# Optimization experiments

Hardware: AMD Instinct MI355X
Metric: run time of the kernel (lower is better)

## Reference

```python
import jax, jax.numpy as jnp
import numpy as np

B, T, D, H = 2, 4096, 768, 12
HD = D // H  # head_dim = 64


def setup_inputs() -> dict:
    key = jax.random.key(0)
    ks = jax.random.split(key, 6)
    s = 0.02
    return {
        "x": jax.random.normal(ks[0], (B, T, D), dtype=jnp.float32),
        "Wq": jax.random.normal(ks[1], (D, D), dtype=jnp.float32) * s,
        "Wk": jax.random.normal(ks[2], (D, D), dtype=jnp.float32) * s,
        "Wv": jax.random.normal(ks[3], (D, D), dtype=jnp.float32) * s,
        "Wo": jax.random.normal(ks[4], (D, D), dtype=jnp.float32) * s,
        "bo": jnp.zeros((D,), dtype=jnp.float32),
    }


def reference(x, Wq, Wk, Wv, Wo, bo):
    b, t, d = x.shape
    # QKV projections (no bias), reshape to [B, H, T, HD]
    def heads(w):
        return (x @ w.T).reshape(b, t, H, HD).transpose(0, 2, 1, 3)
    q, k, v = heads(Wq), heads(Wk), heads(Wv)
    scores = jnp.einsum("bhqd,bhkd->bhqk", q, k)  # [B,H,T,T]
    causal = jnp.tril(jnp.ones((t, t), dtype=bool))
    scores = jnp.where(causal, scores, -jnp.inf)
    attn = jax.nn.softmax(scores / jnp.sqrt(jnp.float32(HD)), axis=-1)
    ctx = jnp.einsum("bhqk,bhkd->bhqd", attn, v)  # [B,H,T,HD]
    ctx = ctx.transpose(0, 2, 1, 3).reshape(b, t, d)
    return ctx @ Wo.T + bo
```

## Files before the change

kernel.cpp:

```cpp
#include <hip/hip_runtime.h>
#include <hip/hip_bf16.h>
#include <cstdint>
#include <cstddef>

#define B_  2
#define T_  4096
#define D_  768
#define H_  12
#define HD_ 64
#define M_  (B_*T_)

#define SCL 0.18033688f

typedef __bf16 bf16x8 __attribute__((ext_vector_type(8)));
typedef float  f32x4  __attribute__((ext_vector_type(4)));
using bf16 = __hip_bfloat16;

__device__ inline float fexp2(float x) {
  float r; asm("v_exp_f32 %0, %1" : "=v"(r) : "v"(x)); return r;
}
__device__ inline uint32_t fu(float x) { union { float f; uint32_t u; } c; c.f = x; return c.u; }
__device__ inline uint32_t pktr(float a, float b) {
  return __builtin_amdgcn_perm(fu(b), fu(a), 0x07060302);
}
#define GLD16(g, l) __builtin_amdgcn_global_load_lds( \
    (const __attribute__((address_space(1))) uint32_t*)(const void*)(g), \
    (__attribute__((address_space(3))) uint32_t*)(void*)(l), 16, 0, 0)

__global__ void cvt_all(const float* __restrict__ x,
                        const float* __restrict__ w0, const float* __restrict__ w1,
                        const float* __restrict__ w2, const float* __restrict__ w3,
                        bf16* __restrict__ xd,
                        bf16* __restrict__ d0, bf16* __restrict__ d1,
                        bf16* __restrict__ d2, bf16* __restrict__ d3) {
  const float* s; bf16* d; int n4;
  switch (blockIdx.y) {
    case 0: s = x;  d = xd; n4 = M_ * D_ / 4; break;
    case 1: s = w0; d = d0; n4 = D_ * D_ / 4; break;
    case 2: s = w1; d = d1; n4 = D_ * D_ / 4; break;
    case 3: s = w2; d = d2; n4 = D_ * D_ / 4; break;
    default: s = w3; d = d3; n4 = D_ * D_ / 4; break;
  }
  int i = blockIdx.x * blockDim.x + threadIdx.x;
  if (i < n4) {
    float4 v = ((const float4*)s)[i];
    union { bf16 o[4]; uint2 u; } pk;
    pk.o[0] = __float2bfloat16(v.x); pk.o[1] = __float2bfloat16(v.y);
    pk.o[2] = __float2bfloat16(v.z); pk.o[3] = __float2bfloat16(v.w);
    *(uint2*)(d + 4 * (size_t)i) = pk.u;
  }
}

__global__ __launch_bounds__(256) void gemm_qkv(const bf16* __restrict__ A,
                                                const bf16* __restrict__ W0,
                                                const bf16* __restrict__ W1,
                                                const bf16* __restrict__ W2,
                                                bf16* __restrict__ O0,
                                                bf16* __restrict__ O1,
                                                bf16* __restrict__ O2t) {
  __shared__ bf16 As[2][4096];
  __shared__ bf16 Bs[2][4096];
  const int z = blockIdx.z;
  const char* Bw = (const char*)((z == 0) ? W0 : ((z == 1) ? W1 : W2));
  const char* Ap = (const char*)A;
  const int t  = threadIdx.x;
  const int m0 = blockIdx.y * 128;
  const int n0 = blockIdx.x * 128;
  const int w = t >> 6, lane = t & 63;
  const int wm = (w >> 1) * 64, wn = (w & 1) * 64;
  const int mi = lane & 15, qd = lane >> 4;

  int aoff[2], boff[2];
  #pragma unroll
  for (int i = 0; i < 2; ++i) {
    int L = i * 256 + t;
    int row = L >> 2, sl = L & 3, c = sl ^ (row & 3);
    aoff[i] = (m0 + row) * 1536 + c * 16;
    boff[i] = (n0 + row) * 1536 + c * 16;
  }
  const int fsw = (qd ^ (mi & 3)) * 8;

  f32x4 acc[4][4] = {};

  #pragma unroll
  for (int i = 0; i < 2; ++i) {
    GLD16(Ap + aoff[i], &As[0][i * 2048 + w * 512]);
    GLD16(Bw + boff[i], &Bs[0][i * 2048 + w * 512]);
  }

  for (int kk = 0; kk < 24; ++kk) {
    __syncthreads();
    const int par = kk & 1;
    if (kk + 1 < 24) {
      const int np = par ^ 1, kb = (kk + 1) * 64;
      #pragma unroll
      for (int i = 0; i < 2; ++i) {
        GLD16(Ap + aoff[i] + kb, &As[np][i * 2048 + w * 512]);
        GLD16(Bw + boff[i] + kb, &Bs[np][i * 2048 + w * 512]);
      }
    }
    bf16x8 af[4], bfr[4];
    #pragma unroll
    for (int mt = 0; mt < 4; ++mt)
      af[mt] = *(const bf16x8*)&As[par][(wm + mt * 16 + mi) * 32 + fsw];
    #pragma unroll
    for (int nt = 0; nt < 4; ++nt)
      bfr[nt] = *(const bf16x8*)&Bs[par][(wn + nt * 16 + mi) * 32 + fsw];
    #pragma unroll
    for (int mt = 0; mt < 4; ++mt)
      #pragma unroll
      for (int nt = 0; nt < 4; ++nt)
        acc[mt][nt] = __builtin_amdgcn_mfma_f32_16x16x32_bf16(af[mt], bfr[nt], acc[mt][nt], 0, 0, 0);
  }

  const float scl = (z == 1) ? SCL : 1.0f;
  bf16* Ob = (z == 0) ? O0 : O1;
  #pragma unroll
  for (int mt = 0; mt < 4; ++mt) {
    #pragma unroll
    for (int nt = 0; nt < 4; ++nt) {
      int gr0 = m0 + wm + mt * 16 + qd * 4;
      int gc  = n0 + wn + nt * 16 + mi;
      if (z == 2) {
        union { bf16 o[4]; uint2 u; } pk;
        #pragma unroll
        for (int r = 0; r < 4; ++r) pk.o[r] = __float2bfloat16(acc[mt][nt][r]);
        int bb = gr0 >> 12, tt = gr0 & 4095;
        *(uint2*)(O2t + (size_t)bb * 768 * 4096 + (size_t)gc * 4096 + tt) = pk.u;
      } else {
        #pragma unroll
        for (int r = 0; r < 4; ++r)
          Ob[(size_t)(gr0 + r) * 768 + gc] = __float2bfloat16(acc[mt][nt][r] * scl);
      }
    }
  }
}

__global__ __launch_bounds__(256) void gemm_out(const bf16* __restrict__ A,
                                                const bf16* __restrict__ Bw0,
                                                float* __restrict__ Cf,
                                                const float* __restrict__ bias) {
  __shared__ bf16 As[2][4096];
  __shared__ bf16 Bs[2][4096];
  const char* Ap = (const char*)A;
  const char* Bw = (const char*)Bw0;
  const int t  = threadIdx.x;
  const int m0 = blockIdx.y * 128;
  const int n0 = blockIdx.x * 128;
  const int w = t >> 6, lane = t & 63;
  const int wm = (w >> 1) * 64, wn = (w & 1) * 64;
  const int mi = lane & 15, qd = lane >> 4;

  int aoff[2], boff[2];
  #pragma unroll
  for (int i = 0; i < 2; ++i) {
    int L = i * 256 + t;
    int row = L >> 2, sl = L & 3, c = sl ^ (row & 3);
    aoff[i] = (m0 + row) * 1536 + c * 16;
    boff[i] = (n0 + row) * 1536 + c * 16;
  }
  const int fsw = (qd ^ (mi & 3)) * 8;

  f32x4 acc[4][4] = {};

  #pragma unroll
  for (int i = 0; i < 2; ++i) {
    GLD16(Ap + aoff[i], &As[0][i * 2048 + w * 512]);
    GLD16(Bw + boff[i], &Bs[0][i * 2048 + w * 512]);
  }

  for (int kk = 0; kk < 24; ++kk) {
    __syncthreads();
    const int par = kk & 1;
    if (kk + 1 < 24) {
      const int np = par ^ 1, kb = (kk + 1) * 64;
      #pragma unroll
      for (int i = 0; i < 2; ++i) {
        GLD16(Ap + aoff[i] + kb, &As[np][i * 2048 + w * 512]);
        GLD16(Bw + boff[i] + kb, &Bs[np][i * 2048 + w * 512]);
      }
    }
    bf16x8 af[4], bfr[4];
    #pragma unroll
    for (int mt = 0; mt < 4; ++mt)
      af[mt] = *(const bf16x8*)&As[par][(wm + mt * 16 + mi) * 32 + fsw];
    #pragma unroll
    for (int nt = 0; nt < 4; ++nt)
      bfr[nt] = *(const bf16x8*)&Bs[par][(wn + nt * 16 + mi) * 32 + fsw];
    #pragma unroll
    for (int mt = 0; mt < 4; ++mt)
      #pragma unroll
      for (int nt = 0; nt < 4; ++nt)
        acc[mt][nt] = __builtin_amdgcn_mfma_f32_16x16x32_bf16(af[mt], bfr[nt], acc[mt][nt], 0, 0, 0);
  }

  #pragma unroll
  for (int mt = 0; mt < 4; ++mt)
    #pragma unroll
    for (int nt = 0; nt < 4; ++nt) {
      int gr0 = m0 + wm + mt * 16 + qd * 4;
      int gc  = n0 + wn + nt * 16 + mi;
      #pragma unroll
      for (int r = 0; r < 4; ++r)
        Cf[(size_t)(gr0 + r) * 768 + gc] = acc[mt][nt][r] + bias[gc];
    }
}

__global__ __launch_bounds__(256) void flash_attn(const bf16* __restrict__ Q,
                                                  const bf16* __restrict__ K,
                                                  const bf16* __restrict__ Vt,
                                                  bf16* __restrict__ ctx) {
  __shared__ bf16 Ks[2][4096];
  __shared__ bf16 Vs[2][4096];
  __shared__ bf16 Pt[4][32 * 72];
  const int t = threadIdx.x;
  const int w = t >> 6, lane = t & 63;
  const int mi = lane & 15, qd = lane >> 4;
  const int bh   = blockIdx.x % 24;
  const int qrev = blockIdx.x / 24;
  const int q0 = T_ - 128 - qrev * 128;
  const int b = bh / H_, h = bh % H_;
  const size_t bTD = (size_t)b * T_ * D_;
  const char* Kp = (const char*)(K  + bTD + (size_t)h * HD_);
  const char* Vp = (const char*)(Vt + (size_t)b * D_ * T_ + (size_t)h * HD_ * T_);
  const int qwmin = q0 + w * 32;

  int vkoff[2], vvoff[2];
  #pragma unroll
  for (int i = 0; i < 2; ++i) {
    int s  = i * 64 + lane;
    int rl = s >> 3, cs = s & 7;
    int c  = cs ^ (rl & 7);
    vkoff[i] = (w * 16 + rl) * 1536 + c * 16;
    vvoff[i] = (w * 16 + rl) * 8192 + c * 16;
  }

  int fidx[4][2];
  #pragma unroll
  for (int jt = 0; jt < 4; ++jt)
    #pragma unroll
    for (int kt = 0; kt < 2; ++kt)
      fidx[jt][kt] = (jt * 16 + mi) * 64 + (((kt * 4 + qd) ^ (mi & 7)) * 8);

  bf16x8 qf[2][2];
  const bf16* Qp = Q + bTD + (size_t)h * HD_;
  #pragma unroll
  for (int qt = 0; qt < 2; ++qt)
    #pragma unroll
    for (int kt = 0; kt < 2; ++kt)
      qf[qt][kt] = *(const bf16x8*)(Qp + (size_t)(qwmin + qt * 16 + mi) * D_ + kt * 32 + qd * 8);

  f32x4 oacc[4][2] = {};
  float lst[2] = {0.f, 0.f};

  const int ntiles = q0 / 64 + 2;

  #pragma unroll
  for (int i = 0; i < 2; ++i) {
    GLD16(Kp + vkoff[i], &Ks[0][w * 1024 + i * 512]);
    GLD16(Vp + vvoff[i], &Vs[0][w * 1024 + i * 512]);
  }

  for (int tt = 0; tt < ntiles; ++tt) {
    __syncthreads();
    const int par = tt & 1;
    if (tt + 1 < ntiles) {
      const size_t j1 = (size_t)(tt + 1) * 64;
      const int np = par ^ 1;
      #pragma unroll
      for (int i = 0; i < 2; ++i) {
        GLD16(Kp + vkoff[i] + j1 * 1536, &Ks[np][w * 1024 + i * 512]);
        GLD16(Vp + vvoff[i] + j1 * 2,    &Vs[np][w * 1024 + i * 512]);
      }
    }
    const int j0 = tt * 64;
    if (j0 > qwmin + 31) continue;

    f32x4 sacc[4][2] = {};
    #pragma unroll
    for (int jt = 0; jt < 4; ++jt)
      #pragma unroll
      for (int kt = 0; kt < 2; ++kt) {
        bf16x8 kf = *(const bf16x8*)&Ks[par][fidx[jt][kt]];
        #pragma unroll
        for (int qt = 0; qt < 2; ++qt)
          sacc[jt][qt] = __builtin_amdgcn_mfma_f32_16x16x32_bf16(kf, qf[qt][kt], sacc[jt][qt], 0, 0, 0);
      }

    if (j0 + 63 > qwmin) {
      #pragma unroll
      for (int jt = 0; jt < 4; ++jt)
        #pragma unroll
        for (int qt = 0; qt < 2; ++qt) {
          int qg = qwmin + qt * 16 + mi;
          #pragma unroll
          for (int r = 0; r < 4; ++r) {
            int jg = j0 + jt * 16 + qd * 4 + r;
            if (jg > qg) sacc[jt][qt][r] = -1e30f;
          }
        }
    }

    #pragma unroll
    for (int jt = 0; jt < 4; ++jt)
      #pragma unroll
      for (int qt = 0; qt < 2; ++qt) {
        float p0 = fexp2(sacc[jt][qt][0]);
        float p1 = fexp2(sacc[jt][qt][1]);
        float p2 = fexp2(sacc[jt][qt][2]);
        float p3 = fexp2(sacc[jt][qt][3]);
        lst[qt] += (p0 + p1) + (p2 + p3);
        union { uint32_t u[2]; uint64_t d; } pw;
        pw.u[0] = pktr(p0, p1);
        pw.u[1] = pktr(p2, p3);
        *(uint64_t*)&Pt[w][(qt * 16 + mi) * 72 + jt * 16 + qd * 4] = pw.d;
      }

    bf16x8 vf[4][2];
    #pragma unroll
    for (int dt = 0; dt < 4; ++dt)
      #pragma unroll
      for (int kt = 0; kt < 2; ++kt)
        vf[dt][kt] = *(const bf16x8*)&Vs[par][fidx[dt][kt]];

    asm volatile("s_waitcnt lgkmcnt(0)" ::: "memory");

    #pragma unroll
    for (int ktp = 0; ktp < 2; ++ktp)
      #pragma unroll
      for (int qt = 0; qt < 2; ++qt) {
        bf16x8 pf = *(const bf16x8*)&Pt[w][(qt * 16 + mi) * 72 + ktp * 32 + qd * 8];
        #pragma unroll
        for (int dt = 0; dt < 4; ++dt)
          oacc[dt][qt] = __builtin_amdgcn_mfma_f32_16x16x32_bf16(vf[dt][ktp], pf, oacc[dt][qt], 0, 0, 0);
      }
  }

  #pragma unroll
  for (int qt = 0; qt < 2; ++qt) {
    float l = lst[qt];
    l += __shfl_xor(l, 16);
    l += __shfl_xor(l, 32);
    float inv = __builtin_amdgcn_rcpf(l);
    int qg = qwmin + qt * 16 + mi;
    bf16* cp = ctx + bTD + (size_t)qg * D_ + h * HD_ + qd * 4;
    #pragma unroll
    for (int dt = 0; dt < 4; ++dt) {
      union { bf16 o[4]; uint2 u; } pko;
      #pragma unroll
      for (int r = 0; r < 4; ++r) pko.o[r] = __float2bfloat16(oacc[dt][qt][r] * inv);
      *(uint2*)(cp + dt * 16) = pko.u;
    }
  }
}

extern "C" void kernel_launch(void* const* d_in, const int* in_sizes, int n_in,
                              void* d_out, int out_size, void* d_ws, size_t ws_size,
                              hipStream_t stream) {
  const float* x  = (const float*)d_in[0];
  const float* Wq = (const float*)d_in[1];
  const float* Wk = (const float*)d_in[2];
  const float* Wv = (const float*)d_in[3];
  const float* Wo = (const float*)d_in[4];
  const float* bo = (const float*)d_in[5];
  float* out = (float*)d_out;

  char* ws = (char*)d_ws;
  const size_t SZ  = (size_t)M_ * D_ * 2;
  const size_t WSZ = (size_t)D_ * D_ * 2;
  bf16* xb   = (bf16*)(ws);
  bf16* Qb   = (bf16*)(ws + 1 * SZ);
  bf16* Kb   = (bf16*)(ws + 2 * SZ);
  bf16* Vtg  = (bf16*)(ws + 3 * SZ);
  bf16* ctxb = (bf16*)(ws + 4 * SZ);
  bf16* Wqb  = (bf16*)(ws + 5 * SZ);
  bf16* Wkb  = (bf16*)(ws + 5 * SZ + 1 * WSZ);
  bf16* Wvb  = (bf16*)(ws + 5 * SZ + 2 * WSZ);
  bf16* Wob  = (bf16*)(ws + 5 * SZ + 3 * WSZ);

  dim3 gcv(M_ * D_ / 4 / 256, 5);
  cvt_all<<<gcv, 256, 0, stream>>>(x, Wq, Wk, Wv, Wo, xb, Wqb, Wkb, Wvb, Wob);

  dim3 gq(D_ / 128, M_ / 128, 3);
  gemm_qkv<<<gq, 256, 0, stream>>>(xb, Wqb, Wkb, Wvb, Qb, Kb, Vtg);

  flash_attn<<<(T_ / 128) * B_ * H_, 256, 0, stream>>>(Qb, Kb, Vtg, ctxb);

  dim3 gg(D_ / 128, M_ / 128);
  gemm_out<<<gg, 256, 0, stream>>>(ctxb, Wob, out, bo);
}
```

Baseline: 266.0 us.

## Keep P in registers via 16x16x16 MFMA, compact convert grid, vectorize GEMM stores

The flash attention P·V product now uses the 16x16x16 bf16 MFMA, whose operand layout matches the score accumulator, so probabilities stay in registers instead of round-tripping through LDS with a wait. The conversion kernel launches a compact 1D grid instead of a 5-row grid in which most weight blocks exit early. The Q/K and output GEMMs swap MFMA operands so each lane holds contiguous output columns, which allows 8-byte bf16 and 16-byte float4 stores with a vectorized bias load. The trade-off is twice as many, smaller MFMA instructions in the P·V loop.

```diff
diff --git a/kernel.cpp b/kernel.cpp
--- a/kernel.cpp
+++ b/kernel.cpp
@@ -14,7 +14,10 @@
 
 typedef __bf16 bf16x8 __attribute__((ext_vector_type(8)));
 typedef float  f32x4  __attribute__((ext_vector_type(4)));
+typedef short  s16x4  __attribute__((ext_vector_type(4)));
 using bf16 = __hip_bfloat16;
+
+#define HAS_MFMA16 __has_builtin(__builtin_amdgcn_mfma_f32_16x16x16bf16_1k)
 
 __device__ inline float fexp2(float x) {
   float r; asm("v_exp_f32 %0, %1" : "=v"(r) : "v"(x)); return r;
@@ -33,22 +36,25 @@
                         bf16* __restrict__ xd,
                         bf16* __restrict__ d0, bf16* __restrict__ d1,
                         bf16* __restrict__ d2, bf16* __restrict__ d3) {
-  const float* s; bf16* d; int n4;
-  switch (blockIdx.y) {
-    case 0: s = x;  d = xd; n4 = M_ * D_ / 4; break;
-    case 1: s = w0; d = d0; n4 = D_ * D_ / 4; break;
-    case 2: s = w1; d = d1; n4 = D_ * D_ / 4; break;
-    case 3: s = w2; d = d2; n4 = D_ * D_ / 4; break;
-    default: s = w3; d = d3; n4 = D_ * D_ / 4; break;
-  }
-  int i = blockIdx.x * blockDim.x + threadIdx.x;
-  if (i < n4) {
-    float4 v = ((const float4*)s)[i];
-    union { bf16 o[4]; uint2 u; } pk;
-    pk.o[0] = __float2bfloat16(v.x); pk.o[1] = __float2bfloat16(v.y);
-    pk.o[2] = __float2bfloat16(v.z); pk.o[3] = __float2bfloat16(v.w);
-    *(uint2*)(d + 4 * (size_t)i) = pk.u;
-  }
+  int blk = blockIdx.x;
+  const float* s; bf16* d; int i;
+  if (blk < 6144) {
+    s = x; d = xd; i = blk * 256 + threadIdx.x;
+  } else {
+    int q = blk - 6144, which = q / 576, rb = q % 576;
+    switch (which) {
+      case 0: s = w0; d = d0; break;
+      case 1: s = w1; d = d1; break;
+      case 2: s = w2; d = d2; break;
+      default: s = w3; d = d3; break;
+    }
+    i = rb * 256 + threadIdx.x;
+  }
+  float4 v = ((const float4*)s)[i];
+  union { bf16 o[4]; uint2 u; } pk;
+  pk.o[0] = __float2bfloat16(v.x); pk.o[1] = __float2bfloat16(v.y);
+  pk.o[2] = __float2bfloat16(v.z); pk.o[3] = __float2bfloat16(v.w);
+  *(uint2*)(d + 4 * (size_t)i) = pk.u;
 }
 
 __global__ __launch_bounds__(256) void gemm_qkv(const bf16* __restrict__ A,
@@ -106,33 +112,48 @@
     #pragma unroll
     for (int nt = 0; nt < 4; ++nt)
       bfr[nt] = *(const bf16x8*)&Bs[par][(wn + nt * 16 + mi) * 32 + fsw];
+    if (z == 2) {
+      #pragma unroll
+      for (int mt = 0; mt < 4; ++mt)
+        #pragma unroll
+        for (int nt = 0; nt < 4; ++nt)
+          acc[mt][nt] = __builtin_amdgcn_mfma_f32_16x16x32_bf16(af[mt], bfr[nt], acc[mt][nt], 0, 0, 0);
+    } else {
+      #pragma unroll
+      for (int mt = 0; mt < 4; ++mt)
+        #pragma unroll
+        for (int nt = 0; nt < 4; ++nt)
+          acc[mt][nt] = __builtin_amdgcn_mfma_f32_16x16x32_bf16(bfr[nt], af[mt], acc[mt][nt], 0, 0, 0);
+    }
+  }
+
+  if (z == 2) {
     #pragma unroll
     for (int mt = 0; mt < 4; ++mt)
       #pragma unroll
-      for (int nt = 0; nt < 4; ++nt)
-        acc[mt][nt] = __builtin_amdgcn_mfma_f32_16x16x32_bf16(af[mt], bfr[nt], acc[mt][nt], 0, 0, 0);
-  }
-
-  const float scl = (z == 1) ? SCL : 1.0f;
-  bf16* Ob = (z == 0) ? O0 : O1;
-  #pragma unroll
-  for (int mt = 0; mt < 4; ++mt) {
-    #pragma unroll
-    for (int nt = 0; nt < 4; ++nt) {
-      int gr0 = m0 + wm + mt * 16 + qd * 4;
-      int gc  = n0 + wn + nt * 16 + mi;
-      if (z == 2) {
+      for (int nt = 0; nt < 4; ++nt) {
+        int gr0 = m0 + wm + mt * 16 + qd * 4;
+        int gc  = n0 + wn + nt * 16 + mi;
         union { bf16 o[4]; uint2 u; } pk;
         #pragma unroll
         for (int r = 0; r < 4; ++r) pk.o[r] = __float2bfloat16(acc[mt][nt][r]);
         int bb = gr0 >> 12, tt = gr0 & 4095;
         *(uint2*)(O2t + (size_t)bb * 768 * 4096 + (size_t)gc * 4096 + tt) = pk.u;
-      } else {
-        #pragma unroll
-        for (int r = 0; r < 4; ++r)
-          Ob[(size_t)(gr0 + r) * 768 + gc] = __float2bfloat16(acc[mt][nt][r] * scl);
-      }
-    }
+      }
+  } else {
+    const float scl = (z == 1) ? SCL : 1.0f;
+    bf16* Ob = (z == 0) ? O0 : O1;
+    #pragma unroll
+    for (int mt = 0; mt < 4; ++mt)
+      #pragma unroll
+      for (int nt = 0; nt < 4; ++nt) {
+        int tkn = m0 + wm + mt * 16 + mi;
+        int f0  = n0 + wn + nt * 16 + qd * 4;
+        union { bf16 o[4]; uint2 u; } pk;
+        #pragma unroll
+        for (int r = 0; r < 4; ++r) pk.o[r] = __float2bfloat16(acc[mt][nt][r] * scl);
+        *(uint2*)(Ob + (size_t)tkn * 768 + f0) = pk.u;
+      }
   }
 }
 
@@ -191,18 +212,20 @@
     for (int mt = 0; mt < 4; ++mt)
       #pragma unroll
       for (int nt = 0; nt < 4; ++nt)
-        acc[mt][nt] = __builtin_amdgcn_mfma_f32_16x16x32_bf16(af[mt], bfr[nt], acc[mt][nt], 0, 0, 0);
+        acc[mt][nt] = __builtin_amdgcn_mfma_f32_16x16x32_bf16(bfr[nt], af[mt], acc[mt][nt], 0, 0, 0);
   }
 
   #pragma unroll
   for (int mt = 0; mt < 4; ++mt)
     #pragma unroll
     for (int nt = 0; nt < 4; ++nt) {
-      int gr0 = m0 + wm + mt * 16 + qd * 4;
-      int gc  = n0 + wn + nt * 16 + mi;
-      #pragma unroll
-      for (int r = 0; r < 4; ++r)
-        Cf[(size_t)(gr0 + r) * 768 + gc] = acc[mt][nt][r] + bias[gc];
+      int tkn = m0 + wm + mt * 16 + mi;
+      int f0  = n0 + wn + nt * 16 + qd * 4;
+      float4 bv = *(const float4*)&bias[f0];
+      float4 o;
+      o.x = acc[mt][nt][0] + bv.x; o.y = acc[mt][nt][1] + bv.y;
+      o.z = acc[mt][nt][2] + bv.z; o.w = acc[mt][nt][3] + bv.w;
+      *(float4*)&Cf[(size_t)tkn * 768 + f0] = o;
     }
 }
 
@@ -212,7 +235,9 @@
                                                   bf16* __restrict__ ctx) {
   __shared__ bf16 Ks[2][4096];
   __shared__ bf16 Vs[2][4096];
+#if !HAS_MFMA16
   __shared__ bf16 Pt[4][32 * 72];
+#endif
   const int t = threadIdx.x;
   const int w = t >> 6, lane = t & 63;
   const int mi = lane & 15, qd = lane >> 4;
@@ -242,6 +267,13 @@
     for (int kt = 0; kt < 2; ++kt)
       fidx[jt][kt] = (jt * 16 + mi) * 64 + (((kt * 4 + qd) ^ (mi & 7)) * 8);
 
+  int vidx[4][4];
+  #pragma unroll
+  for (int dt = 0; dt < 4; ++dt)
+    #pragma unroll
+    for (int jt = 0; jt < 4; ++jt)
+      vidx[dt][jt] = (dt * 16 + mi) * 64 + ((2 * jt + (qd >> 1)) ^ (mi & 7)) * 8 + (qd & 1) * 4;
+
   bf16x8 qf[2][2];
   const bf16* Qp = Q + bTD + (size_t)h * HD_;
   #pragma unroll
@@ -301,6 +333,7 @@
         }
     }
 
+    union { uint32_t u[2]; uint64_t d; s16x4 s; } pf[4][2];
     #pragma unroll
     for (int jt = 0; jt < 4; ++jt)
       #pragma unroll
@@ -310,30 +343,47 @@
         float p2 = fexp2(sacc[jt][qt][2]);
         float p3 = fexp2(sacc[jt][qt][3]);
         lst[qt] += (p0 + p1) + (p2 + p3);
-        union { uint32_t u[2]; uint64_t d; } pw;
-        pw.u[0] = pktr(p0, p1);
-        pw.u[1] = pktr(p2, p3);
-        *(uint64_t*)&Pt[w][(qt * 16 + mi) * 72 + jt * 16 + qd * 4] = pw.d;
-      }
-
+        pf[jt][qt].u[0] = pktr(p0, p1);
+        pf[jt][qt].u[1] = pktr(p2, p3);
+      }
+
+#if HAS_MFMA16
+    s16x4 vf4[4][4];
+    #pragma unroll
+    for (int dt = 0; dt < 4; ++dt)
+      #pragma unroll
+      for (int jt = 0; jt < 4; ++jt)
+        vf4[dt][jt] = *(const s16x4*)&Vs[par][vidx[dt][jt]];
+    #pragma unroll
+    for (int qt = 0; qt < 2; ++qt)
+      #pragma unroll
+      for (int dt = 0; dt < 4; ++dt)
+        #pragma unroll
+        for (int jt = 0; jt < 4; ++jt)
+          oacc[dt][qt] = __builtin_amdgcn_mfma_f32_16x16x16bf16_1k(vf4[dt][jt], pf[jt][qt].s, oacc[dt][qt], 0, 0, 0);
+#else
+    #pragma unroll
+    for (int jt = 0; jt < 4; ++jt)
+      #pragma unroll
+      for (int qt = 0; qt < 2; ++qt)
+        *(uint64_t*)&Pt[w][(qt * 16 + mi) * 72 + jt * 16 + qd * 4] = pf[jt][qt].d;
     bf16x8 vf[4][2];
     #pragma unroll
     for (int dt = 0; dt < 4; ++dt)
       #pragma unroll
       for (int kt = 0; kt < 2; ++kt)
         vf[dt][kt] = *(const bf16x8*)&Vs[par][fidx[dt][kt]];
-
     asm volatile("s_waitcnt lgkmcnt(0)" ::: "memory");
-
     #pragma unroll
     for (int ktp = 0; ktp < 2; ++ktp)
       #pragma unroll
       for (int qt = 0; qt < 2; ++qt) {
-        bf16x8 pf = *(const bf16x8*)&Pt[w][(qt * 16 + mi) * 72 + ktp * 32 + qd * 8];
+        bf16x8 pfx = *(const bf16x8*)&Pt[w][(qt * 16 + mi) * 72 + ktp * 32 + qd * 8];
         #pragma unroll
         for (int dt = 0; dt < 4; ++dt)
-          oacc[dt][qt] = __builtin_amdgcn_mfma_f32_16x16x32_bf16(vf[dt][ktp], pf, oacc[dt][qt], 0, 0, 0);
-      }
+          oacc[dt][qt] = __builtin_amdgcn_mfma_f32_16x16x32_bf16(vf[dt][ktp], pfx, oacc[dt][qt], 0, 0, 0);
+      }
+#endif
   }
 
   #pragma unroll
@@ -378,8 +428,7 @@
   bf16* Wvb  = (bf16*)(ws + 5 * SZ + 2 * WSZ);
   bf16* Wob  = (bf16*)(ws + 5 * SZ + 3 * WSZ);
 
-  dim3 gcv(M_ * D_ / 4 / 256, 5);
-  cvt_all<<<gcv, 256, 0, stream>>>(x, Wq, Wk, Wv, Wo, xb, Wqb, Wkb, Wvb, Wob);
+  cvt_all<<<6144 + 4 * 576, 256, 0, stream>>>(x, Wq, Wk, Wv, Wo, xb, Wqb, Wkb, Wvb, Wob);
 
   dim3 gq(D_ / 128, M_ / 128, 3);
   gemm_qkv<<<gq, 256, 0, stream>>>(xb, Wqb, Wkb, Wvb, Qb, Kb, Vtg);
```

New measurement: 281.4 us. 1.06x slower.

## Flatten grids, transpose GEMM operands for vector stores, widen attention to 512 threads

Applied to the files above, without the earlier changes.

The conversion kernel now uses a compact 1D grid, replacing the 5-row grid that wasted blocks on the small weight matrices. The QKV and output GEMMs swap operand roles (weights as A, activations as B) so each lane's accumulator holds four contiguous features, which allows packed 64-bit bf16 and float4 stores instead of scalar ones. Flash attention moves to 512 threads with 8 waves of 16 query rows each, halving per-wave register state and the K/V staging per thread. The cost is more waves sharing each K/V tile and less reuse of each K/V fragment per MFMA.

```diff
diff --git a/kernel.cpp b/kernel.cpp
--- a/kernel.cpp
+++ b/kernel.cpp
@@ -33,25 +33,28 @@
                         bf16* __restrict__ xd,
                         bf16* __restrict__ d0, bf16* __restrict__ d1,
                         bf16* __restrict__ d2, bf16* __restrict__ d3) {
-  const float* s; bf16* d; int n4;
-  switch (blockIdx.y) {
-    case 0: s = x;  d = xd; n4 = M_ * D_ / 4; break;
-    case 1: s = w0; d = d0; n4 = D_ * D_ / 4; break;
-    case 2: s = w1; d = d1; n4 = D_ * D_ / 4; break;
-    case 3: s = w2; d = d2; n4 = D_ * D_ / 4; break;
-    default: s = w3; d = d3; n4 = D_ * D_ / 4; break;
-  }
-  int i = blockIdx.x * blockDim.x + threadIdx.x;
-  if (i < n4) {
-    float4 v = ((const float4*)s)[i];
-    union { bf16 o[4]; uint2 u; } pk;
-    pk.o[0] = __float2bfloat16(v.x); pk.o[1] = __float2bfloat16(v.y);
-    pk.o[2] = __float2bfloat16(v.z); pk.o[3] = __float2bfloat16(v.w);
-    *(uint2*)(d + 4 * (size_t)i) = pk.u;
-  }
-}
-
-__global__ __launch_bounds__(256) void gemm_qkv(const bf16* __restrict__ A,
+  int blk = blockIdx.x;
+  const float* s; bf16* d; int i;
+  if (blk < 6144) {
+    s = x; d = xd; i = blk * 256 + threadIdx.x;
+  } else {
+    int q = blk - 6144, which = q / 576, rb = q % 576;
+    switch (which) {
+      case 0: s = w0; d = d0; break;
+      case 1: s = w1; d = d1; break;
+      case 2: s = w2; d = d2; break;
+      default: s = w3; d = d3; break;
+    }
+    i = rb * 256 + threadIdx.x;
+  }
+  float4 v = ((const float4*)s)[i];
+  union { bf16 o[4]; uint2 u; } pk;
+  pk.o[0] = __float2bfloat16(v.x); pk.o[1] = __float2bfloat16(v.y);
+  pk.o[2] = __float2bfloat16(v.z); pk.o[3] = __float2bfloat16(v.w);
+  *(uint2*)(d + 4 * (size_t)i) = pk.u;
+}
+
+__global__ __launch_bounds__(256) void gemm_qkv(const bf16* __restrict__ x,
                                                 const bf16* __restrict__ W0,
                                                 const bf16* __restrict__ W1,
                                                 const bf16* __restrict__ W2,
@@ -60,14 +63,18 @@
                                                 bf16* __restrict__ O2t) {
   __shared__ bf16 As[2][4096];
   __shared__ bf16 Bs[2][4096];
-  const int z = blockIdx.z;
-  const char* Bw = (const char*)((z == 0) ? W0 : ((z == 1) ? W1 : W2));
-  const char* Ap = (const char*)A;
-  const int t  = threadIdx.x;
-  const int m0 = blockIdx.y * 128;
-  const int n0 = blockIdx.x * 128;
+  const int flat = blockIdx.x;
+  const int by = flat / 18;
+  const int rr = flat % 18;
+  const int z  = rr / 6;
+  const int bx = rr % 6;
+  const bf16* Wz = (z == 0) ? W0 : ((z == 1) ? W1 : W2);
+  const char* Ap; const char* Bp; int a0, b0;
+  if (z == 2) { Ap = (const char*)x;  a0 = by * 128; Bp = (const char*)Wz; b0 = bx * 128; }
+  else        { Ap = (const char*)Wz; a0 = bx * 128; Bp = (const char*)x;  b0 = by * 128; }
+  const int t = threadIdx.x;
   const int w = t >> 6, lane = t & 63;
-  const int wm = (w >> 1) * 64, wn = (w & 1) * 64;
+  const int wa = (w >> 1) * 64, wb = (w & 1) * 64;
   const int mi = lane & 15, qd = lane >> 4;
 
   int aoff[2], boff[2];
@@ -75,8 +82,8 @@
   for (int i = 0; i < 2; ++i) {
     int L = i * 256 + t;
     int row = L >> 2, sl = L & 3, c = sl ^ (row & 3);
-    aoff[i] = (m0 + row) * 1536 + c * 16;
-    boff[i] = (n0 + row) * 1536 + c * 16;
+    aoff[i] = (a0 + row) * 1536 + c * 16;
+    boff[i] = (b0 + row) * 1536 + c * 16;
   }
   const int fsw = (qd ^ (mi & 3)) * 8;
 
@@ -85,7 +92,7 @@
   #pragma unroll
   for (int i = 0; i < 2; ++i) {
     GLD16(Ap + aoff[i], &As[0][i * 2048 + w * 512]);
-    GLD16(Bw + boff[i], &Bs[0][i * 2048 + w * 512]);
+    GLD16(Bp + boff[i], &Bs[0][i * 2048 + w * 512]);
   }
 
   for (int kk = 0; kk < 24; ++kk) {
@@ -96,59 +103,66 @@
       #pragma unroll
       for (int i = 0; i < 2; ++i) {
         GLD16(Ap + aoff[i] + kb, &As[np][i * 2048 + w * 512]);
-        GLD16(Bw + boff[i] + kb, &Bs[np][i * 2048 + w * 512]);
+        GLD16(Bp + boff[i] + kb, &Bs[np][i * 2048 + w * 512]);
       }
     }
     bf16x8 af[4], bfr[4];
     #pragma unroll
-    for (int mt = 0; mt < 4; ++mt)
-      af[mt] = *(const bf16x8*)&As[par][(wm + mt * 16 + mi) * 32 + fsw];
-    #pragma unroll
-    for (int nt = 0; nt < 4; ++nt)
-      bfr[nt] = *(const bf16x8*)&Bs[par][(wn + nt * 16 + mi) * 32 + fsw];
-    #pragma unroll
-    for (int mt = 0; mt < 4; ++mt)
-      #pragma unroll
-      for (int nt = 0; nt < 4; ++nt)
-        acc[mt][nt] = __builtin_amdgcn_mfma_f32_16x16x32_bf16(af[mt], bfr[nt], acc[mt][nt], 0, 0, 0);
-  }
-
-  const float scl = (z == 1) ? SCL : 1.0f;
-  bf16* Ob = (z == 0) ? O0 : O1;
-  #pragma unroll
-  for (int mt = 0; mt < 4; ++mt) {
-    #pragma unroll
-    for (int nt = 0; nt < 4; ++nt) {
-      int gr0 = m0 + wm + mt * 16 + qd * 4;
-      int gc  = n0 + wn + nt * 16 + mi;
-      if (z == 2) {
+    for (int at = 0; at < 4; ++at)
+      af[at] = *(const bf16x8*)&As[par][(wa + at * 16 + mi) * 32 + fsw];
+    #pragma unroll
+    for (int bt = 0; bt < 4; ++bt)
+      bfr[bt] = *(const bf16x8*)&Bs[par][(wb + bt * 16 + mi) * 32 + fsw];
+    #pragma unroll
+    for (int at = 0; at < 4; ++at)
+      #pragma unroll
+      for (int bt = 0; bt < 4; ++bt)
+        acc[at][bt] = __builtin_amdgcn_mfma_f32_16x16x32_bf16(af[at], bfr[bt], acc[at][bt], 0, 0, 0);
+  }
+
+  if (z == 2) {
+    #pragma unroll
+    for (int at = 0; at < 4; ++at)
+      #pragma unroll
+      for (int bt = 0; bt < 4; ++bt) {
+        int gr = a0 + wa + at * 16 + qd * 4;
+        int gc = b0 + wb + bt * 16 + mi;
         union { bf16 o[4]; uint2 u; } pk;
         #pragma unroll
-        for (int r = 0; r < 4; ++r) pk.o[r] = __float2bfloat16(acc[mt][nt][r]);
-        int bb = gr0 >> 12, tt = gr0 & 4095;
+        for (int r = 0; r < 4; ++r) pk.o[r] = __float2bfloat16(acc[at][bt][r]);
+        int bb = gr >> 12, tt = gr & 4095;
         *(uint2*)(O2t + (size_t)bb * 768 * 4096 + (size_t)gc * 4096 + tt) = pk.u;
-      } else {
+      }
+  } else {
+    const float scl = (z == 1) ? SCL : 1.0f;
+    bf16* Ob = (z == 0) ? O0 : O1;
+    #pragma unroll
+    for (int at = 0; at < 4; ++at)
+      #pragma unroll
+      for (int bt = 0; bt < 4; ++bt) {
+        int f0  = a0 + wa + at * 16 + qd * 4;
+        int tkn = b0 + wb + bt * 16 + mi;
+        union { bf16 o[4]; uint2 u; } pk;
         #pragma unroll
-        for (int r = 0; r < 4; ++r)
-          Ob[(size_t)(gr0 + r) * 768 + gc] = __float2bfloat16(acc[mt][nt][r] * scl);
-      }
-    }
-  }
-}
-
-__global__ __launch_bounds__(256) void gemm_out(const bf16* __restrict__ A,
-                                                const bf16* __restrict__ Bw0,
+        for (int r = 0; r < 4; ++r) pk.o[r] = __float2bfloat16(acc[at][bt][r] * scl);
+        *(uint2*)(Ob + (size_t)tkn * 768 + f0) = pk.u;
+      }
+  }
+}
+
+__global__ __launch_bounds__(256) void gemm_out(const bf16* __restrict__ ctx,
+                                                const bf16* __restrict__ Wo,
                                                 float* __restrict__ Cf,
                                                 const float* __restrict__ bias) {
   __shared__ bf16 As[2][4096];
   __shared__ bf16 Bs[2][4096];
-  const char* Ap = (const char*)A;
-  const char* Bw = (const char*)Bw0;
-  const int t  = threadIdx.x;
-  const int m0 = blockIdx.y * 128;
-  const int n0 = blockIdx.x * 128;
+  const int flat = blockIdx.x;
+  const int by = flat / 6, bx = flat % 6;
+  const char* Ap = (const char*)Wo;  const int a0 = bx * 128;
+  const char* Bp = (const char*)ctx; const int b0 = by * 128;
+  const int t = threadIdx.x;
   const int w = t >> 6, lane = t & 63;
-  const int wm = (w >> 1) * 64, wn = (w & 1) * 64;
+  const int wa = (w >> 1) * 64, wb = (w & 1) * 64;
   const int mi = lane & 15, qd = lane >> 4;
 
   int aoff[2], boff[2];
@@ -156,8 +170,8 @@
   for (int i = 0; i < 2; ++i) {
     int L = i * 256 + t;
     int row = L >> 2, sl = L & 3, c = sl ^ (row & 3);
-    aoff[i] = (m0 + row) * 1536 + c * 16;
-    boff[i] = (n0 + row) * 1536 + c * 16;
+    aoff[i] = (a0 + row) * 1536 + c * 16;
+    boff[i] = (b0 + row) * 1536 + c * 16;
   }
   const int fsw = (qd ^ (mi & 3)) * 8;
 
@@ -166,7 +180,7 @@
   #pragma unroll
   for (int i = 0; i < 2; ++i) {
     GLD16(Ap + aoff[i], &As[0][i * 2048 + w * 512]);
-    GLD16(Bw + boff[i], &Bs[0][i * 2048 + w * 512]);
+    GLD16(Bp + boff[i], &Bs[0][i * 2048 + w * 512]);
   }
 
   for (int kk = 0; kk < 24; ++kk) {
@@ -177,42 +191,44 @@
       #pragma unroll
       for (int i = 0; i < 2; ++i) {
         GLD16(Ap + aoff[i] + kb, &As[np][i * 2048 + w * 512]);
-        GLD16(Bw + boff[i] + kb, &Bs[np][i * 2048 + w * 512]);
+        GLD16(Bp + boff[i] + kb, &Bs[np][i * 2048 + w * 512]);
       }
     }
     bf16x8 af[4], bfr[4];
     #pragma unroll
-    for (int mt = 0; mt < 4; ++mt)
-      af[mt] = *(const bf16x8*)&As[par][(wm + mt * 16 + mi) * 32 + fsw];
-    #pragma unroll
-    for (int nt = 0; nt < 4; ++nt)
-      bfr[nt] = *(const bf16x8*)&Bs[par][(wn + nt * 16 + mi) * 32 + fsw];
-    #pragma unroll
-    for (int mt = 0; mt < 4; ++mt)
-      #pragma unroll
-      for (int nt = 0; nt < 4; ++nt)
-        acc[mt][nt] = __builtin_amdgcn_mfma_f32_16x16x32_bf16(af[mt], bfr[nt], acc[mt][nt], 0, 0, 0);
-  }
-
-  #pragma unroll
-  for (int mt = 0; mt < 4; ++mt)
-    #pragma unroll
-    for (int nt = 0; nt < 4; ++nt) {
-      int gr0 = m0 + wm + mt * 16 + qd * 4;
-      int gc  = n0 + wn + nt * 16 + mi;
-      #pragma unroll
-      for (int r = 0; r < 4; ++r)
-        Cf[(size_t)(gr0 + r) * 768 + gc] = acc[mt][nt][r] + bias[gc];
-    }
-}
-
-__global__ __launch_bounds__(256) void flash_attn(const bf16* __restrict__ Q,
-                                                  const bf16* __restrict__ K,
-                                                  const bf16* __restrict__ Vt,
-                                                  bf16* __restrict__ ctx) {
+    for (int at = 0; at < 4; ++at)
+      af[at] = *(const bf16x8*)&As[par][(wa + at * 16 + mi) * 32 + fsw];
+    #pragma unroll
+    for (int bt = 0; bt < 4; ++bt)
+      bfr[bt] = *(const bf16x8*)&Bs[par][(wb + bt * 16 + mi) * 32 + fsw];
+    #pragma unroll
+    for (int at = 0; at < 4; ++at)
+      #pragma unroll
+      for (int bt = 0; bt < 4; ++bt)
+        acc[at][bt] = __builtin_amdgcn_mfma_f32_16x16x32_bf16(af[at], bfr[bt], acc[at][bt], 0, 0, 0);
+  }
+
+  #pragma unroll
+  for (int at = 0; at < 4; ++at)
+    #pragma unroll
+    for (int bt = 0; bt < 4; ++bt) {
+      int f0  = a0 + wa + at * 16 + qd * 4;
+      int tkn = b0 + wb + bt * 16 + mi;
+      float4 bv = *(const float4*)&bias[f0];
+      float4 o;
+      o.x = acc[at][bt][0] + bv.x; o.y = acc[at][bt][1] + bv.y;
+      o.z = acc[at][bt][2] + bv.z; o.w = acc[at][bt][3] + bv.w;
+      *(float4*)&Cf[(size_t)tkn * 768 + f0] = o;
+    }
+}
+
+__global__ __launch_bounds__(512, 4) void flash_attn(const bf16* __restrict__ Q,
+                                                     const bf16* __restrict__ K,
+                                                     const bf16* __restrict__ Vt,
+                                                     bf16* __restrict__ ctx) {
   __shared__ bf16 Ks[2][4096];
   __shared__ bf16 Vs[2][4096];
-  __shared__ bf16 Pt[4][32 * 72];
+  __shared__ bf16 Pt[8][16 * 72];
   const int t = threadIdx.x;
   const int w = t >> 6, lane = t & 63;
   const int mi = lane & 15, qd = lane >> 4;
@@ -223,17 +239,11 @@
   const size_t bTD = (size_t)b * T_ * D_;
   const char* Kp = (const char*)(K  + bTD + (size_t)h * HD_);
   const char* Vp = (const char*)(Vt + (size_t)b * D_ * T_ + (size_t)h * HD_ * T_);
-  const int qwmin = q0 + w * 32;
-
-  int vkoff[2], vvoff[2];
-  #pragma unroll
-  for (int i = 0; i < 2; ++i) {
-    int s  = i * 64 + lane;
-    int rl = s >> 3, cs = s & 7;
-    int c  = cs ^ (rl & 7);
-    vkoff[i] = (w * 16 + rl) * 1536 + c * 16;
-    vvoff[i] = (w * 16 + rl) * 8192 + c * 16;
-  }
+  const int qw = q0 + w * 16;
+
+  const int rl = t >> 3, c = (t & 7) ^ (rl & 7);
+  const int vkoff = rl * 1536 + c * 16;
+  const int vvoff = rl * 8192 + c * 16;
 
   int fidx[4][2];
   #pragma unroll
@@ -242,24 +252,18 @@
     for (int kt = 0; kt < 2; ++kt)
       fidx[jt][kt] = (jt * 16 + mi) * 64 + (((kt * 4 + qd) ^ (mi & 7)) * 8);
 
-  bf16x8 qf[2][2];
+  bf16x8 qf[2];
   const bf16* Qp = Q + bTD + (size_t)h * HD_;
   #pragma unroll
-  for (int qt = 0; qt < 2; ++qt)
-    #pragma unroll
-    for (int kt = 0; kt < 2; ++kt)
-      qf[qt][kt] = *(const bf16x8*)(Qp + (size_t)(qwmin + qt * 16 + mi) * D_ + kt * 32 + qd * 8);
-
-  f32x4 oacc[4][2] = {};
-  float lst[2] = {0.f, 0.f};
-
+  for (int kt = 0; kt < 2; ++kt)
+    qf[kt] = *(const bf16x8*)(Qp + (size_t)(qw + mi) * D_ + kt * 32 + qd * 8);
+
+  f32x4 oacc[4] = {};
+  float lst = 0.f;
   const int ntiles = q0 / 64 + 2;
 
-  #pragma unroll
-  for (int i = 0; i < 2; ++i) {
-    GLD16(Kp + vkoff[i], &Ks[0][w * 1024 + i * 512]);
-    GLD16(Vp + vvoff[i], &Vs[0][w * 1024 + i * 512]);
-  }
+  GLD16(Kp + vkoff, &Ks[0][w * 512]);
+  GLD16(Vp + vvoff, &Vs[0][w * 512]);
 
   for (int tt = 0; tt < ntiles; ++tt) {
     __syncthreads();
@@ -267,90 +271,70 @@
     if (tt + 1 < ntiles) {
       const size_t j1 = (size_t)(tt + 1) * 64;
       const int np = par ^ 1;
-      #pragma unroll
-      for (int i = 0; i < 2; ++i) {
-        GLD16(Kp + vkoff[i] + j1 * 1536, &Ks[np][w * 1024 + i * 512]);
-        GLD16(Vp + vvoff[i] + j1 * 2,    &Vs[np][w * 1024 + i * 512]);
-      }
+      GLD16(Kp + vkoff + j1 * 1536, &Ks[np][w * 512]);
+      GLD16(Vp + vvoff + j1 * 2,    &Vs[np][w * 512]);
     }
     const int j0 = tt * 64;
-    if (j0 > qwmin + 31) continue;
-
-    f32x4 sacc[4][2] = {};
+    if (j0 > qw + 15) continue;
+
+    f32x4 sacc[4] = {};
     #pragma unroll
     for (int jt = 0; jt < 4; ++jt)
       #pragma unroll
       for (int kt = 0; kt < 2; ++kt) {
         bf16x8 kf = *(const bf16x8*)&Ks[par][fidx[jt][kt]];
-        #pragma unroll
-        for (int qt = 0; qt < 2; ++qt)
-          sacc[jt][qt] = __builtin_amdgcn_mfma_f32_16x16x32_bf16(kf, qf[qt][kt], sacc[jt][qt], 0, 0, 0);
-      }
-
-    if (j0 + 63 > qwmin) {
+        sacc[jt] = __builtin_amdgcn_mfma_f32_16x16x32_bf16(kf, qf[kt], sacc[jt], 0, 0, 0);
+      }
+
+    if (j0 + 63 > qw) {
+      const int qg = qw + mi;
       #pragma unroll
       for (int jt = 0; jt < 4; ++jt)
         #pragma unroll
-        for (int qt = 0; qt < 2; ++qt) {
-          int qg = qwmin + qt * 16 + mi;
-          #pragma unroll
-          for (int r = 0; r < 4; ++r) {
-            int jg = j0 + jt * 16 + qd * 4 + r;
-            if (jg > qg) sacc[jt][qt][r] = -1e30f;
-          }
+        for (int r = 0; r < 4; ++r) {
+          int jg = j0 + jt * 16 + qd * 4 + r;
+          if (jg > qg) sacc[jt][r] = -1e30f;
         }
     }
 
     #pragma unroll
-    for (int jt = 0; jt < 4; ++jt)
-      #pragma unroll
-      for (int qt = 0; qt < 2; ++qt) {
-        float p0 = fexp2(sacc[jt][qt][0]);
-        float p1 = fexp2(sacc[jt][qt][1]);
-        float p2 = fexp2(sacc[jt][qt][2]);
-        float p3 = fexp2(sacc[jt][qt][3]);
-        lst[qt] += (p0 + p1) + (p2 + p3);
-        union { uint32_t u[2]; uint64_t d; } pw;
-        pw.u[0] = pktr(p0, p1);
-        pw.u[1] = pktr(p2, p3);
-        *(uint64_t*)&Pt[w][(qt * 16 + mi) * 72 + jt * 16 + qd * 4] = pw.d;
-      }
-
-    bf16x8 vf[4][2];
-    #pragma unroll
-    for (int dt = 0; dt < 4; ++dt)
-      #pragma unroll
-      for (int kt = 0; kt < 2; ++kt)
-        vf[dt][kt] = *(const bf16x8*)&Vs[par][fidx[dt][kt]];
+    for (int jt = 0; jt < 4; ++jt) {
+      float p0 = fexp2(sacc[jt][0]);
+      float p1 = fexp2(sacc[jt][1]);
+      float p2 = fexp2(sacc[jt][2]);
+      float p3 = fexp2(sacc[jt][3]);
+      lst += (p0 + p1) + (p2 + p3);
+      union { uint32_t u[2]; uint64_t d; } pw;
+      pw.u[0] = pktr(p0, p1);
+      pw.u[1] = pktr(p2, p3);
+      *(uint64_t*)&Pt[w][mi * 72 + jt * 16 + qd * 4] = pw.d;
+    }
 
     asm volatile("s_waitcnt lgkmcnt(0)" ::: "memory");
 
     #pragma unroll
-    for (int ktp = 0; ktp < 2; ++ktp)
-      #pragma unroll
-      for (int qt = 0; qt < 2; ++qt) {
-        bf16x8 pf = *(const bf16x8*)&Pt[w][(qt * 16 + mi) * 72 + ktp * 32 + qd * 8];
-        #pragma unroll
-        for (int dt = 0; dt < 4; ++dt)
-          oacc[dt][qt] = __builtin_amdgcn_mfma_f32_16x16x32_bf16(vf[dt][ktp], pf, oacc[dt][qt], 0, 0, 0);
-      }
-  }
-
-  #pragma unroll
-  for (int qt = 0; qt < 2; ++qt) {
-    float l = lst[qt];
-    l += __shfl_xor(l, 16);
-    l += __shfl_xor(l, 32);
-    float inv = __builtin_amdgcn_rcpf(l);
-    int qg = qwmin + qt * 16 + mi;
-    bf16* cp = ctx + bTD + (size_t)qg * D_ + h * HD_ + qd * 4;
-    #pragma unroll
-    for (int dt = 0; dt < 4; ++dt) {
-      union { bf16 o[4]; uint2 u; } pko;
-      #pragma unroll
-      for (int r = 0; r < 4; ++r) pko.o[r] = __float2bfloat16(oacc[dt][qt][r] * inv);
-      *(uint2*)(cp + dt * 16) = pko.u;
-    }
+    for (int ktp = 0; ktp < 2; ++ktp) {
+      bf16x8 pfx = *(const bf16x8*)&Pt[w][mi * 72 + ktp * 32 + qd * 8];
+      #pragma unroll
+      for (int dt = 0; dt < 4; ++dt) {
+        bf16x8 vf = *(const bf16x8*)&Vs[par][fidx[dt][ktp]];
+        oacc[dt] = __builtin_amdgcn_mfma_f32_16x16x32_bf16(vf, pfx, oacc[dt], 0, 0, 0);
+      }
+    }
+  }
+
+  float l = lst;
+  l += __shfl_xor(l, 16);
+  l += __shfl_xor(l, 32);
+  float inv = __builtin_amdgcn_rcpf(l);
+  const int qg = qw + mi;
+  bf16* cp = ctx + bTD + (size_t)qg * D_ + h * HD_ + qd * 4;
+  #pragma unroll
+  for (int dt = 0; dt < 4; ++dt) {
+    union { bf16 o[4]; uint2 u; } pko;
+    #pragma unroll
+    for (int r = 0; r < 4; ++r) pko.o[r] = __float2bfloat16(oacc[dt][r] * inv);
+    *(uint2*)(cp + dt * 16) = pko.u;
   }
 }
 
@@ -378,14 +362,11 @@
   bf16* Wvb  = (bf16*)(ws + 5 * SZ + 2 * WSZ);
   bf16* Wob  = (bf16*)(ws + 5 * SZ + 3 * WSZ);
 
-  dim3 gcv(M_ * D_ / 4 / 256, 5);
-  cvt_all<<<gcv, 256, 0, stream>>>(x, Wq, Wk, Wv, Wo, xb, Wqb, Wkb, Wvb, Wob);
-
-  dim3 gq(D_ / 128, M_ / 128, 3);
-  gemm_qkv<<<gq, 256, 0, stream>>>(xb, Wqb, Wkb, Wvb, Qb, Kb, Vtg);
-
-  flash_attn<<<(T_ / 128) * B_ * H_, 256, 0, stream>>>(Qb, Kb, Vtg, ctxb);
-
-  dim3 gg(D_ / 128, M_ / 128);
-  gemm_out<<<gg, 256, 0, stream>>>(ctxb, Wob, out, bo);
-}
+  cvt_all<<<6144 + 4 * 576, 256, 0, stream>>>(x, Wq, Wk, Wv, Wo, xb, Wqb, Wkb, Wvb, Wob);
+
+  gemm_qkv<<<1152, 256, 0, stream>>>(xb, Wqb, Wkb, Wvb, Qb, Kb, Vtg);
+
+  flash_attn<<<(T_ / 128) * B_ * H_, 512, 0, stream>>>(Qb, Kb, Vtg, ctxb);
+
+  gemm_out<<<384, 256, 0, stream>>>(ctxb, Wob, out, bo);
+}
```

Result: faster. 246.1 us (-7.5%).
